# Kernel optimization log

Measured on AMD Instinct MI355X. Metric: run time of the kernel, lower is better.

Reference implementation:

```python
import jax, jax.numpy as jnp
import numpy as np

B, N, D, H = 1, 4096, 1024, 16
K = D // H
ROPE_BASE = 10000.0


def _rope_cos_sin(n, k, base, dtype):
    # GPT-NeoX style rotary embedding: inv_freq over even dims, emb = cat(freqs, freqs)
    inv_freq = 1.0 / (base ** (jnp.arange(0, k, 2, dtype=jnp.float32) / k))  # [K/2]
    pos = jnp.arange(n, dtype=jnp.float32)
    freqs = pos[:, None] * inv_freq[None, :]              # [N, K/2]
    emb = jnp.concatenate([freqs, freqs], axis=-1)        # [N, K]
    return jnp.cos(emb).astype(dtype), jnp.sin(emb).astype(dtype)


def _rotate_half(x):
    x1, x2 = jnp.split(x, 2, axis=-1)
    return jnp.concatenate([-x2, x1], axis=-1)


def setup_inputs() -> dict:
    key = jax.random.key(0)
    kx, kq, ko = jax.random.split(key, 3)
    x = jax.random.normal(kx, (B, N, D), dtype=jnp.float32)
    # torch Linear weights: [out_features, in_features], y = x @ W^T
    w_qkv = jax.random.normal(kq, (3 * H * K, D), dtype=jnp.float32) / np.sqrt(D)
    w_out = jax.random.normal(ko, (D, D), dtype=jnp.float32) / np.sqrt(D)
    return {"x": x, "w_qkv": w_qkv, "w_out": w_out}


def reference(x, w_qkv, w_out):
    b, n, d = x.shape
    qkv = jnp.einsum('bnd,ed->bne', x, w_qkv).reshape(b, n, 3, H, K)
    q, k, v = qkv[:, :, 0], qkv[:, :, 1], qkv[:, :, 2]   # [B, N, H, K]
    cos, sin = _rope_cos_sin(n, K, ROPE_BASE, x.dtype)    # [N, K]
    cos = cos[None, :, None, :]
    sin = sin[None, :, None, :]
    q = q * cos + _rotate_half(q) * sin
    k = k * cos + _rotate_half(k) * sin
    # explicit O(N^2) score matrix, as in the original module
    scores = jnp.einsum('bnhk,bmhk->bnhm', q, k) / np.sqrt(K).astype(x.dtype)
    causal_mask = jnp.tril(jnp.ones((n, n), dtype=bool))  # [N, M]
    scores = jnp.where(causal_mask[None, :, None, :], scores, jnp.finfo(x.dtype).min)
    probs = jax.nn.softmax(scores, axis=-1)
    attn = jnp.einsum('bnhm,bmhk->bnhk', probs, v).reshape(b, n, d)
    return jnp.einsum('bnd,ed->bne', attn, w_out)
```

## Files before the change

kernel.cpp:

```cpp
#include <hip/hip_runtime.h>
#include <hip/hip_bf16.h>
#include <math.h>

#define N_SEQ 4096
#define DIM   1024
#define NHEAD 16
#define HDIM  64
#define E3    3072

typedef short bf16x8 __attribute__((ext_vector_type(8)));
typedef float f32x4  __attribute__((ext_vector_type(4)));
typedef unsigned int u32;

#if __has_builtin(__builtin_amdgcn_exp2f)
#define EXP2(x) __builtin_amdgcn_exp2f(x)
#else
#define EXP2(x) exp2f(x)
#endif

__device__ __forceinline__ float bf2f(unsigned short u) {
    union { unsigned int i; float f; } x; x.i = ((unsigned int)u) << 16; return x.f;
}
__device__ __forceinline__ unsigned short f2bf(float f) {
    union { float f; unsigned int i; } x; x.f = f;
    unsigned int r = x.i + 0x7FFF + ((x.i >> 16) & 1);
    return (unsigned short)(r >> 16);
}
__device__ __forceinline__ unsigned short f2bf_fast(float f) {
    union { float f; unsigned int i; } x; x.f = f;
    return (unsigned short)((x.i + 0x8000u) >> 16);
}
__device__ __forceinline__ f32x4 mfma16(bf16x8 a, bf16x8 b, f32x4 c) {
    return __builtin_amdgcn_mfma_f32_16x16x32_bf16(a, b, c, 0, 0, 0);
}
__device__ __forceinline__ void gload_lds16(const unsigned short* g, unsigned short* l) {
    __builtin_amdgcn_global_load_lds(
        (const __attribute__((address_space(1))) u32*)g,
        (__attribute__((address_space(3))) u32*)l, 16, 0, 0);
}

__device__ __forceinline__ int probe_isf32(const unsigned short* __restrict__ X) {
    __shared__ int cnt;
    if (threadIdx.x == 0) cnt = 0;
    __syncthreads();
    int bad = 0;
    for (int i = threadIdx.x; i < 4096; i += 256) {
        float v = bf2f(X[i]);
        if (!(fabsf(v) < 1e10f)) bad = 1;
    }
    if (bad) atomicAdd(&cnt, 1);
    __syncthreads();
    return cnt > 0;
}

__global__ __launch_bounds__(256)
void prep_kernel(const void* __restrict__ X, const void* __restrict__ Wq,
                 const void* __restrict__ Wo,
                 unsigned short* __restrict__ Xb, unsigned short* __restrict__ Wqb,
                 unsigned short* __restrict__ Wob,
                 float4* __restrict__ Rt,
                 int* __restrict__ flag)
{
    const int ti = blockIdx.x * blockDim.x + threadIdx.x;
    if (ti < N_SEQ * 16) {
        const int n = ti >> 4, f = ti & 15;
        const float i0 = powf(10000.f, -((float)f)        * (1.f/32.f));
        const float i1 = powf(10000.f, -((float)(f + 16)) * (1.f/32.f));
        float s0, c0, s1, c1;
        sincosf((float)n * i0, &s0, &c0);
        sincosf((float)n * i1, &s1, &c1);
        Rt[ti] = (float4){c0, c1, s0, s1};
    }

    const int isf32 = probe_isf32((const unsigned short*)X);
    if (blockIdx.x == 0 && threadIdx.x == 0) *flag = isf32;
    if (!isf32) return;

    const int nX4  = (N_SEQ * DIM) >> 2;
    const int nWq4 = (E3 * DIM) >> 2;
    const int nWo4 = (DIM * DIM) >> 2;
    const int total = nX4 + nWq4 + nWo4;
    const int stride = gridDim.x * blockDim.x;
    for (int i = blockIdx.x * blockDim.x + threadIdx.x; i < total; i += stride) {
        const float4* src; ushort4* dst; int j = i;
        if (j < nX4)                { src = (const float4*)X  + j;  dst = (ushort4*)Xb  + j; }
        else if ((j -= nX4) < nWq4) { src = (const float4*)Wq + j;  dst = (ushort4*)Wqb + j; }
        else { j -= nWq4;             src = (const float4*)Wo + j;  dst = (ushort4*)Wob + j; }
        float4 v = *src;
        ushort4 u;
        u.x = f2bf(v.x); u.y = f2bf(v.y); u.z = f2bf(v.z); u.w = f2bf(v.w);
        *dst = u;
    }
}

__global__ __launch_bounds__(256)
void qkv_mfma_kernel(const void* __restrict__ Xo, const unsigned short* __restrict__ Xc,
                     const void* __restrict__ Wo_, const unsigned short* __restrict__ Wc,
                     const int* __restrict__ flag,
                     const float4* __restrict__ Rt,
                     unsigned short* __restrict__ Qf,
                     unsigned short* __restrict__ Kf,
                     unsigned short* __restrict__ Vf)
{
    __shared__ __align__(16) unsigned short SMEM[4][4096];

    const int isf32 = *flag;
    const unsigned short* Xb = isf32 ? Xc : (const unsigned short*)Xo;
    const unsigned short* Wb = isf32 ? Wc : (const unsigned short*)Wo_;

    const int tid  = threadIdx.x;
    const int lane = tid & 63;
    const int wave = tid >> 6;
    const int wr = wave >> 1, wc = wave & 1;
    const int lm = lane & 15, q4 = lane >> 4;
    const int rbase = blockIdx.y * 128;
    const int cbase = blockIdx.x * 128;

    const int srow = wave * 16 + (lane >> 2);
    const int scol = (lane & 3) * 8;

    const unsigned short* xsrc = Xb + (size_t)(rbase + srow) * DIM + scol;
    const unsigned short* wsrc = Wb + (size_t)(cbase + srow) * DIM + scol;
    const int la = (wr*64 + lm)*32 + q4*8;
    const int lb = (wc*64 + lm)*32 + q4*8;

    f32x4 acc[4][4];
    #pragma unroll
    for (int i = 0; i < 4; ++i)
        #pragma unroll
        for (int j = 0; j < 4; ++j) acc[i][j] = (f32x4){0.f, 0.f, 0.f, 0.f};

    #define QSTAGE(buf)                                                             \
        {                                                                           \
            _Pragma("unroll")                                                       \
            for (int j = 0; j < 2; ++j) {                                           \
                gload_lds16(xsrc + (size_t)j*64*DIM, &SMEM[buf][j*2048 + wave*512]);   \
                gload_lds16(wsrc + (size_t)j*64*DIM, &SMEM[2+buf][j*2048 + wave*512]); \
            }                                                                       \
            xsrc += 32; wsrc += 32;                                                 \
        }

    QSTAGE(0)
    for (int it = 0; it < DIM/32; ++it) {
        const int cur = it & 1;
        __syncthreads();
        if (it + 1 < DIM/32) QSTAGE(cur ^ 1)

        bf16x8 a[4], b[4];
        #pragma unroll
        for (int mi = 0; mi < 4; ++mi)
            a[mi] = *(const bf16x8*)&SMEM[cur][la + mi*512];
        #pragma unroll
        for (int ni = 0; ni < 4; ++ni)
            b[ni] = *(const bf16x8*)&SMEM[2+cur][lb + ni*512];
        #pragma unroll
        for (int mi = 0; mi < 4; ++mi)
            #pragma unroll
            for (int ni = 0; ni < 4; ++ni)
                acc[mi][ni] = mfma16(a[mi], b[ni], acc[mi][ni]);
    }
    #undef QSTAGE

    __syncthreads();

    const int ecol = cbase + wc * 64;
    const int part = ecol >> 10;
    const int h    = (ecol >> 6) & 15;
    unsigned short* ep = &SMEM[0][0] + wave*4096;

    if (part == 2) {
        #pragma unroll
        for (int mh = 0; mh < 2; ++mh) {
            #pragma unroll
            for (int mi2 = 0; mi2 < 2; ++mi2) {
                const int mi = mh*2 + mi2;
                #pragma unroll
                for (int r = 0; r < 4; ++r) {
                    const int n31 = mi2*16 + q4*4 + r;
                    #pragma unroll
                    for (int ni = 0; ni < 4; ++ni)
                        ep[(ni*16 + lm)*40 + n31] = f2bf(acc[mi][ni][r]);
                }
            }
            const int nb = rbase + wr*64 + mh*32;
            const size_t vb = (((size_t)h*128 + (nb >> 5)) << 11) + (size_t)lane*8;
            #pragma unroll
            for (int ni = 0; ni < 4; ++ni) {
                const bf16x8 fr = *(const bf16x8*)(ep + (ni*16 + lm)*40 + q4*8);
                *(bf16x8*)(Vf + vb + (size_t)ni*512) = fr;
            }
        }
    } else {
        unsigned short* dst = (part == 0) ? Qf : Kf;
        const float scl = (part == 0) ? 0.180336884f : 1.0f;
        #pragma unroll
        for (int mi = 0; mi < 4; ++mi) {
            const int tn = rbase + wr*64 + mi*16;
            #pragma unroll
            for (int r = 0; r < 4; ++r) {
                const int n = tn + q4*4 + r;
                const float4 t = Rt[(n << 4) + lm];
                const int row = (q4*4 + r)*72;
                ep[row + lm]      = f2bf((acc[mi][0][r]*t.x - acc[mi][2][r]*t.z) * scl);
                ep[row + lm + 16] = f2bf((acc[mi][1][r]*t.y - acc[mi][3][r]*t.w) * scl);
                ep[row + lm + 32] = f2bf((acc[mi][2][r]*t.x + acc[mi][0][r]*t.z) * scl);
                ep[row + lm + 48] = f2bf((acc[mi][3][r]*t.y + acc[mi][1][r]*t.w) * scl);
            }
            const size_t tb = (((size_t)(h*256 + (tn >> 4))) << 10) + (size_t)lane*8;
            #pragma unroll
            for (int c = 0; c < 2; ++c) {
                const bf16x8 fr = *(const bf16x8*)(ep + lm*72 + c*32 + q4*8);
                *(bf16x8*)(dst + tb + (size_t)c*512) = fr;
            }
        }
    }
}

__global__ __launch_bounds__(512, 2)
void attn_mfma_kernel(const unsigned short* __restrict__ Qf,
                      const unsigned short* __restrict__ Kf,
                      const unsigned short* __restrict__ Vf,
                      unsigned short* __restrict__ Attn)
{
    __shared__ __align__(16) unsigned short P16[8][2][16][40];
    __shared__ __align__(16) float Ox[4][16][64];
    __shared__ float Lx[4][16];

    const int tid  = threadIdx.x;
    const int lane = tid & 63;
    const int wave = tid >> 6;
    const int q4 = lane >> 4, lm = lane & 15;
    const int qh = wave >> 1;
    const int kh = wave & 1;

    const int h = blockIdx.x & 15;
    const int p = blockIdx.x >> 4;
    const int qwA = (p << 6) + (qh << 4);
    const int qwB = ((63 - p) << 6) + (qh << 4);
    const int ntA = p + 1;
    const int ntB = 64 - p;

    const unsigned short* qpA = Qf + (((size_t)(h*256 + (qwA >> 4))) << 10) + (size_t)lane * 8;
    const unsigned short* qpB = Qf + (((size_t)(h*256 + (qwB >> 4))) << 10) + (size_t)lane * 8;
    bf16x8 aqA[2], aqB[2];
    #pragma unroll
    for (int d = 0; d < 2; ++d) {
        aqA[d] = *(const bf16x8*)(qpA + d*512);
        aqB[d] = *(const bf16x8*)(qpB + d*512);
    }

    float lA[4], lB[4];
    f32x4 oA[4], oB[4];
    #pragma unroll
    for (int r = 0; r < 4; ++r) { lA[r] = 0.f; lB[r] = 0.f; }
    #pragma unroll
    for (int dc = 0; dc < 4; ++dc) {
        oA[dc] = (f32x4){0.f, 0.f, 0.f, 0.f};
        oB[dc] = (f32x4){0.f, 0.f, 0.f, 0.f};
    }

    const size_t hb = ((size_t)h) << 18;
    const unsigned short* kc = Kf + hb + (size_t)(kh*2048) + (size_t)lane*8;
    const unsigned short* vc = Vf + hb + (size_t)(kh*2048) + (size_t)lane*8;

    unsigned short* pwA  = &P16[wave][0][0][0];
    unsigned short* pwB  = &P16[wave][1][0][0];
    unsigned short* pwaA = pwA + (4*q4)*40 + lm;
    unsigned short* pwaB = pwB + (4*q4)*40 + lm;
    const unsigned short* parA = pwA + lm*40 + q4*8;
    const unsigned short* parB = pwB + lm*40 + q4*8;

    for (int it = 0; it < ntB; ++it) {
        const int kt = it << 6;
        const int doA = (it < ntA);

        bf16x8 bk[2][2];
        bk[0][0] = *(const bf16x8*)(kc);
        bk[0][1] = *(const bf16x8*)(kc + 512);
        bk[1][0] = *(const bf16x8*)(kc + 1024);
        bk[1][1] = *(const bf16x8*)(kc + 1536);

        bf16x8 bv[4];
        #pragma unroll
        for (int dc = 0; dc < 4; ++dc)
            bv[dc] = *(const bf16x8*)(vc + dc*512);

        f32x4 sB[2], sA[2];
        #pragma unroll
        for (int ki = 0; ki < 2; ++ki) {
            f32x4 z = (f32x4){0.f, 0.f, 0.f, 0.f};
            z = mfma16(aqB[0], bk[ki][0], z);
            sB[ki] = mfma16(aqB[1], bk[ki][1], z);
        }
        if (doA) {
            #pragma unroll
            for (int ki = 0; ki < 2; ++ki) {
                f32x4 z = (f32x4){0.f, 0.f, 0.f, 0.f};
                z = mfma16(aqA[0], bk[ki][0], z);
                sA[ki] = mfma16(aqA[1], bk[ki][1], z);
            }
        }

        if (kt + 32*kh + 31 > qwB) {
            #pragma unroll
            for (int ki = 0; ki < 2; ++ki) {
                const int key = kt + 32*kh + 16*ki + lm;
                const int qq = qwB + 4*q4;
                #pragma unroll
                for (int r = 0; r < 4; ++r)
                    if (key > qq + r) sB[ki][r] = -INFINITY;
            }
        }

        #pragma unroll
        for (int ki = 0; ki < 2; ++ki)
            #pragma unroll
            for (int r = 0; r < 4; ++r) {
                const float pb = EXP2(sB[ki][r]);
                lB[r] += pb;
                pwaB[r*40 + ki*16] = f2bf_fast(pb);
            }

        if (doA) {
            if (kt + 32*kh + 31 > qwA) {
                #pragma unroll
                for (int ki = 0; ki < 2; ++ki) {
                    const int key = kt + 32*kh + 16*ki + lm;
                    const int qq = qwA + 4*q4;
                    #pragma unroll
                    for (int r = 0; r < 4; ++r)
                        if (key > qq + r) sA[ki][r] = -INFINITY;
                }
            }
            #pragma unroll
            for (int ki = 0; ki < 2; ++ki)
                #pragma unroll
                for (int r = 0; r < 4; ++r) {
                    const float pa = EXP2(sA[ki][r]);
                    lA[r] += pa;
                    pwaA[r*40 + ki*16] = f2bf_fast(pa);
                }
        }

        {
            const bf16x8 paB = *(const bf16x8*)(parB);
            #pragma unroll
            for (int dc = 0; dc < 4; ++dc)
                oB[dc] = mfma16(paB, bv[dc], oB[dc]);
        }
        if (doA) {
            const bf16x8 paA = *(const bf16x8*)(parA);
            #pragma unroll
            for (int dc = 0; dc < 4; ++dc)
                oA[dc] = mfma16(paA, bv[dc], oA[dc]);
        }

        kc += 4096; vc += 4096;
    }

    #pragma unroll
    for (int r = 0; r < 4; ++r) {
        float a = lA[r], b = lB[r];
        #pragma unroll
        for (int mk = 1; mk <= 8; mk <<= 1) {
            a += __shfl_xor(a, mk);
            b += __shfl_xor(b, mk);
        }
        lA[r] = a; lB[r] = b;
    }

    if (kh == 1) {
        #pragma unroll
        for (int r = 0; r < 4; ++r) {
            const int qq = 4*q4 + r;
            #pragma unroll
            for (int dc = 0; dc < 4; ++dc)
                Ox[qh][qq][16*dc + lm] = oA[dc][r];
            if (lm == 0) Lx[qh][qq] = lA[r];
        }
    }
    __syncthreads();
    if (kh == 0) {
        #pragma unroll
        for (int r = 0; r < 4; ++r) {
            const int qq = 4*q4 + r;
            const float inv = 1.f / (lA[r] + Lx[qh][qq]);
            const size_t row = (size_t)(qwA + qq) * DIM + (h << 6) + lm;
            #pragma unroll
            for (int dc = 0; dc < 4; ++dc) {
                const float v = oA[dc][r] + Ox[qh][qq][16*dc + lm];
                Attn[row + 16*dc] = f2bf(v * inv);
            }
        }
    }
    __syncthreads();
    if (kh == 1) {
        #pragma unroll
        for (int r = 0; r < 4; ++r) {
            const int qq = 4*q4 + r;
            #pragma unroll
            for (int dc = 0; dc < 4; ++dc)
                Ox[qh][qq][16*dc + lm] = oB[dc][r];
            if (lm == 0) Lx[qh][qq] = lB[r];
        }
    }
    __syncthreads();
    if (kh == 0) {
        #pragma unroll
        for (int r = 0; r < 4; ++r) {
            const int qq = 4*q4 + r;
            const float inv = 1.f / (lB[r] + Lx[qh][qq]);
            const size_t row = (size_t)(qwB + qq) * DIM + (h << 6) + lm;
            #pragma unroll
            for (int dc = 0; dc < 4; ++dc) {
                const float v = oB[dc][r] + Ox[qh][qq][16*dc + lm];
                Attn[row + 16*dc] = f2bf(v * inv);
            }
        }
    }
}

__global__ __launch_bounds__(256)
void out_mfma_kernel(const unsigned short* __restrict__ Ab,
                     const void* __restrict__ Wo_, const unsigned short* __restrict__ Wc,
                     const int* __restrict__ flag,
                     void* __restrict__ Out)
{
    __shared__ unsigned short As[2][4096];
    __shared__ unsigned short Bs[2][2048];

    const int isf32 = *flag;
    const unsigned short* Wb = isf32 ? Wc : (const unsigned short*)Wo_;

    const int tid  = threadIdx.x;
    const int lane = tid & 63;
    const int wave = tid >> 6;
    const int lm = lane & 15, q4 = lane >> 4;
    const int rbase = blockIdx.y * 128;
    const int cbase = blockIdx.x * 64;

    const int srow16 = lane >> 2;
    const int scol = (lane & 3) * 8;

    const unsigned short* asrc = Ab + (size_t)(rbase + wave*32 + srow16) * DIM + scol;
    const unsigned short* bsrc = Wb + (size_t)(cbase + wave*16 + srow16) * DIM + scol;
    const int la = (wave*32 + lm)*32 + q4*8;
    const int lb = lm*32 + q4*8;

    f32x4 acc[2][4];
    #pragma unroll
    for (int i = 0; i < 2; ++i)
        #pragma unroll
        for (int j = 0; j < 4; ++j) acc[i][j] = (f32x4){0.f, 0.f, 0.f, 0.f};

    #define OSTAGE(buf)                                                          \
        {                                                                        \
            _Pragma("unroll")                                                    \
            for (int j = 0; j < 2; ++j)                                          \
                gload_lds16(asrc + (size_t)j*16*DIM, &As[buf][(wave*32 + j*16)*32]); \
            gload_lds16(bsrc, &Bs[buf][(wave*16)*32]);                           \
            asrc += 32; bsrc += 32;                                              \
        }

    OSTAGE(0)
    for (int it = 0; it < DIM/32; ++it) {
        const int cur = it & 1;
        __syncthreads();
        if (it + 1 < DIM/32) OSTAGE(cur ^ 1)

        bf16x8 a[2], b[4];
        #pragma unroll
        for (int mi = 0; mi < 2; ++mi)
            a[mi] = *(const bf16x8*)&As[cur][la + mi*512];
        #pragma unroll
        for (int ni = 0; ni < 4; ++ni)
            b[ni] = *(const bf16x8*)&Bs[cur][lb + ni*512];
        #pragma unroll
        for (int mi = 0; mi < 2; ++mi)
            #pragma unroll
            for (int ni = 0; ni < 4; ++ni)
                acc[mi][ni] = mfma16(a[mi], b[ni], acc[mi][ni]);
    }
    #undef OSTAGE

    #pragma unroll
    for (int mi = 0; mi < 2; ++mi)
        #pragma unroll
        for (int r = 0; r < 4; ++r) {
            const size_t n = rbase + wave*32 + mi*16 + q4*4 + r;
            #pragma unroll
            for (int ni = 0; ni < 4; ++ni) {
                const size_t e = cbase + ni*16 + lm;
                const float v = acc[mi][ni][r];
                if (isf32) ((float*)Out)[n * DIM + e] = v;
                else       ((unsigned short*)Out)[n * DIM + e] = f2bf(v);
            }
        }
}

extern "C" void kernel_launch(void* const* d_in, const int* in_sizes, int n_in,
                              void* d_out, int out_size, void* d_ws, size_t ws_size,
                              hipStream_t stream) {
    const void* X    = d_in[0];
    const void* Wqkv = d_in[1];
    const void* Wout = d_in[2];

    int* flag = (int*)d_ws;
    unsigned short* base = (unsigned short*)((char*)d_ws + 256);
    const size_t nX = (size_t)N_SEQ * DIM;
    const size_t nWq = (size_t)E3 * DIM;
    const size_t nWo = (size_t)DIM * DIM;
    unsigned short* Xb  = base;
    unsigned short* Wqb = Xb + nX;
    unsigned short* Wob = Wqb + nWq;
    unsigned short* Qf  = Wob + nWo;
    unsigned short* Kf  = Qf + nX;
    unsigned short* Vf  = Kf + nX;
    unsigned short* At  = Vf + nX;
    float4* Rt = (float4*)(At + nX);

    prep_kernel<<<768, 256, 0, stream>>>(X, Wqkv, Wout, Xb, Wqb, Wob, Rt, flag);
    qkv_mfma_kernel<<<dim3(E3 / 128, N_SEQ / 128), 256, 0, stream>>>(X, Xb, Wqkv, Wqb, flag, Rt, Qf, Kf, Vf);
    attn_mfma_kernel<<<dim3(NHEAD * 32), 512, 0, stream>>>(Qf, Kf, Vf, At);
    out_mfma_kernel<<<dim3(DIM / 64, N_SEQ / 128), 256, 0, stream>>>(At, Wout, Wob, flag, d_out);
}
```

Measured before the change: 211.9 us.

## Stage K/V tiles into double-buffered LDS via direct global-to-LDS loads

Each 64-key K/V tile is now loaded once per block into a double-buffered LDS area using global-to-LDS loads, with each wave fetching one slice. Waves then read their fragments from LDS. Before, the four query-half waves each loaded the same tile from global memory. This removes redundant global/L2 traffic and prefetches the next tile while the current one is processed. The cost is a block-wide barrier every iteration and 32KB of extra LDS per block, which could limit occupancy.

```diff
diff --git a/kernel.cpp b/kernel.cpp
--- a/kernel.cpp
+++ b/kernel.cpp
@@ -222,6 +222,8 @@
                       const unsigned short* __restrict__ Vf,
                       unsigned short* __restrict__ Attn)
 {
+    __shared__ __align__(16) unsigned short Ks[2][4096];
+    __shared__ __align__(16) unsigned short Vs[2][4096];
     __shared__ __align__(16) unsigned short P16[8][2][16][40];
     __shared__ __align__(16) float Ox[4][16][64];
     __shared__ float Lx[4][16];
@@ -260,8 +262,10 @@
     }
 
     const size_t hb = ((size_t)h) << 18;
-    const unsigned short* kc = Kf + hb + (size_t)(kh*2048) + (size_t)lane*8;
-    const unsigned short* vc = Vf + hb + (size_t)(kh*2048) + (size_t)lane*8;
+    const unsigned short* kg = Kf + hb + wave*512 + (size_t)lane*8;
+    const unsigned short* vg = Vf + hb + wave*512 + (size_t)lane*8;
+
+    const int kbase = kh*2048 + lane*8;
 
     unsigned short* pwA  = &P16[wave][0][0][0];
     unsigned short* pwB  = &P16[wave][1][0][0];
@@ -270,20 +274,34 @@
     const unsigned short* parA = pwA + lm*40 + q4*8;
     const unsigned short* parB = pwB + lm*40 + q4*8;
 
+    #define STAGE(buf)                                   \
+        {                                                \
+            gload_lds16(kg, &Ks[buf][wave*512]);         \
+            gload_lds16(vg, &Vs[buf][wave*512]);         \
+            kg += 4096; vg += 4096;                      \
+        }
+
+    STAGE(0)
+
     for (int it = 0; it < ntB; ++it) {
         const int kt = it << 6;
+        const int cur = it & 1;
         const int doA = (it < ntA);
 
+        __syncthreads();
+        if (it + 1 < ntB) STAGE(cur ^ 1)
+
+        const unsigned short* kcl = &Ks[cur][kbase];
+        const unsigned short* vcl = &Vs[cur][kbase];
         bf16x8 bk[2][2];
-        bk[0][0] = *(const bf16x8*)(kc);
-        bk[0][1] = *(const bf16x8*)(kc + 512);
-        bk[1][0] = *(const bf16x8*)(kc + 1024);
-        bk[1][1] = *(const bf16x8*)(kc + 1536);
-
+        bk[0][0] = *(const bf16x8*)(kcl);
+        bk[0][1] = *(const bf16x8*)(kcl + 512);
+        bk[1][0] = *(const bf16x8*)(kcl + 1024);
+        bk[1][1] = *(const bf16x8*)(kcl + 1536);
         bf16x8 bv[4];
         #pragma unroll
         for (int dc = 0; dc < 4; ++dc)
-            bv[dc] = *(const bf16x8*)(vc + dc*512);
+            bv[dc] = *(const bf16x8*)(vcl + dc*512);
 
         f32x4 sB[2], sA[2];
         #pragma unroll
@@ -354,9 +372,8 @@
             for (int dc = 0; dc < 4; ++dc)
                 oA[dc] = mfma16(paA, bv[dc], oA[dc]);
         }
-
-        kc += 4096; vc += 4096;
-    }
+    }
+    #undef STAGE
 
     #pragma unroll
     for (int r = 0; r < 4; ++r) {
```

Result: slower. 234.8 us (+10.8%).
